# Kernel optimization log

Measured on AMD Instinct MI355X. Metric: run time of the kernel, lower is better.

## Reference

```python
import jax, jax.numpy as jnp
import numpy as np

B, S, K, D = 512, 64, 8, 16
NE, NR, NU = 2_000_000, 64, 10_000
NSTEPS, NUNITS, NITER = 100, 128, 2


def _alpha_schedule():
    # betas = sigmoid(linspace(-6,6)) * (0.005 - 1e-5) + 1e-5; alphas_prod = cumprod(1-betas)
    betas = jax.nn.sigmoid(jnp.linspace(-6.0, 6.0, NSTEPS)) * (0.005 - 1e-5) + 1e-5
    aprod = jnp.cumprod(1.0 - betas)
    return jnp.sqrt(aprod), jnp.sqrt(1.0 - aprod)


def _forward(usr_emb, ent_emb, rel_emb, agg_W, agg_b, fc1_W, fc1_b, fc2_W, fc2_b,
             mlp_W1, mlp_b1, mlp_W2, mlp_b2, mlp_W3, mlp_b3, mlp_W4, mlp_b4,
             step_emb1, step_emb2, step_emb3, noise_e, u, v, click_seq, adj_ent, adj_rel, t):
    user = usr_emb[u]                                   # [B,D]
    # --- diffusion branch: x = x0*sqrt(abar_t) + e*sqrt(1-abar_t), then MLP with step-emb adds
    abar_sqrt, ombar_sqrt = _alpha_schedule()
    x = user * abar_sqrt[t][:, None] + noise_e * ombar_sqrt[t][:, None]
    for Wl, bl, se in ((mlp_W1, mlp_b1, step_emb1), (mlp_W2, mlp_b2, step_emb2), (mlp_W3, mlp_b3, step_emb3)):
        x = jax.nn.relu(x @ Wl + bl + se[t])            # [B,128]
    diff_out = x @ mlp_W4 + mlp_b4                      # [B,D]
    # --- multi-hop neighbor gather (entities/relations per hop)
    e0 = click_seq                                      # [B,S]
    e1 = adj_ent[e0]                                    # [B,S,K]
    e2 = adj_ent[e1].reshape(B, S, K * K)               # [B,S,K*K]
    r0 = adj_rel[e0]                                    # [B,S,K]
    r1 = adj_rel[e1].reshape(B, S, K * K)               # [B,S,K*K]
    ev = [ent_emb[e0][:, :, None, :], ent_emb[e1], ent_emb[e2]]  # [B,S,1,D],[B,S,K,D],[B,S,K*K,D]
    rv = [rel_emb[r0], rel_emb[r1]]

    def aggregate(self_v, neigh_v, rel_v, act):
        # KGCN sum-aggregator: user-relation score softmax over neighbors, weighted sum, linear, act
        scores = jnp.mean(user[:, None, None, None, :] * rel_v, axis=-1)   # [B,S,n,K]
        p = jax.nn.softmax(scores, axis=-1)
        neigh_agg = jnp.einsum('bsnk,bsnkd->bsnd', p, neigh_v)             # [B,S,n,D]
        return act((self_v + neigh_agg) @ agg_W + agg_b)

    for i in range(NITER):
        act = jnp.tanh if i == NITER - 1 else jax.nn.sigmoid
        nxt = []
        for hop in range(NITER - i):
            n_self = ev[hop].shape[2]
            nv = ev[hop + 1].reshape(B, S, n_self, K, D)
            relv = rv[hop].reshape(B, S, n_self, K, D)
            nxt.append(aggregate(ev[hop], nv, relv, act))
        ev = nxt
    item_emb = jax.nn.relu(ev[0].reshape(B, S, D))      # relu applied twice in source == once
    trans = item_emb                                    # Transform treated as identity (code unavailable)
    s_sum = jax.nn.relu(jnp.sum(trans, axis=1))         # [B,D]
    s_max = jax.nn.relu(jnp.max(trans, axis=1))         # [B,D]
    fusion = jnp.concatenate([s_sum, s_max], axis=1)    # [B,2D]
    feat = jax.nn.relu(jax.nn.relu(fusion @ fc1_W + fc1_b) @ fc2_W + fc2_b)  # [B,D]
    outs = jax.nn.sigmoid(jnp.sum(feat * ent_emb[v], axis=1))               # [B]
    return jnp.concatenate([outs[:, None], diff_out], axis=1)               # [B,1+D]


def setup_inputs() -> dict:
    key = jax.random.key(0)
    ks = iter(jax.random.split(key, 32))
    nrm = lambda shape, s: jax.random.normal(next(ks), shape, dtype=jnp.float32) * s
    zf = lambda shape: jnp.zeros(shape, dtype=jnp.float32)
    ri = lambda shape, hi: jax.random.randint(next(ks), shape, 0, hi, dtype=jnp.int32)
    return {
        'usr_emb': nrm((NU, D), 0.1), 'ent_emb': nrm((NE, D), 0.1), 'rel_emb': nrm((NR, D), 0.1),
        'agg_W': nrm((D, D), 0.25), 'agg_b': zf((D,)),
        'fc1_W': nrm((2 * D, 64), 0.18), 'fc1_b': zf((64,)),
        'fc2_W': nrm((64, D), 0.125), 'fc2_b': zf((D,)),
        'mlp_W1': nrm((D, NUNITS), 0.25), 'mlp_b1': zf((NUNITS,)),
        'mlp_W2': nrm((NUNITS, NUNITS), 0.09), 'mlp_b2': zf((NUNITS,)),
        'mlp_W3': nrm((NUNITS, NUNITS), 0.09), 'mlp_b3': zf((NUNITS,)),
        'mlp_W4': nrm((NUNITS, D), 0.09), 'mlp_b4': zf((D,)),
        'step_emb1': nrm((NSTEPS, NUNITS), 0.1), 'step_emb2': nrm((NSTEPS, NUNITS), 0.1),
        'step_emb3': nrm((NSTEPS, NUNITS), 0.1),
        'noise_e': jax.random.normal(next(ks), (B, D), dtype=jnp.float32),
        'u': ri((B,), NU), 'v': ri((B,), NE), 'click_seq': ri((B, S), NE),
        'adj_ent': ri((NE, K), NE), 'adj_rel': ri((NE, K), NR), 't': ri((B,), NSTEPS),
    }


def reference(usr_emb, ent_emb, rel_emb, agg_W, agg_b, fc1_W, fc1_b, fc2_W, fc2_b,
              mlp_W1, mlp_b1, mlp_W2, mlp_b2, mlp_W3, mlp_b3, mlp_W4, mlp_b4,
              step_emb1, step_emb2, step_emb3, noise_e, u, v, click_seq, adj_ent, adj_rel, t):
    return _forward(usr_emb, ent_emb, rel_emb, agg_W, agg_b, fc1_W, fc1_b, fc2_W, fc2_b,
                    mlp_W1, mlp_b1, mlp_W2, mlp_b2, mlp_W3, mlp_b3, mlp_W4, mlp_b4,
                    step_emb1, step_emb2, step_emb3, noise_e, u, v, click_seq, adj_ent, adj_rel, t)
```

## Files before the change

kernel.cpp:

```cpp
#include <hip/hip_runtime.h>
#include <math.h>

namespace {
constexpr int B = 512, S = 64, K = 8, D = 16, NR = 64, NSTEPS = 100, NUNITS = 128;
}

__global__ void k_sched(float* __restrict__ sa, float* __restrict__ so) {
    int i = threadIdx.x;
    if (i < NSTEPS) {
        float prod = 1.0f;
        for (int jj = 0; jj <= i; ++jj) {
            float x = -6.0f + (float)jj * (12.0f / 99.0f);
            float sig = 1.0f / (1.0f + expf(-x));
            float beta = sig * (0.005f - 1e-5f) + 1e-5f;
            prod *= (1.0f - beta);
        }
        sa[i] = sqrtf(prod);
        so[i] = sqrtf(1.0f - prod);
    }
}

__global__ void k_userrel(const float* __restrict__ usr_emb,
                          const float* __restrict__ rel_emb,
                          const int* __restrict__ u,
                          float* __restrict__ w) {
    int b = blockIdx.x, r = threadIdx.x;
    const float* ur = usr_emb + (long)u[b] * D;
    const float* rr = rel_emb + r * D;
    float s = 0.f;
#pragma unroll
    for (int d = 0; d < D; ++d) s += ur[d] * rr[d];
    w[b * NR + r] = s * (1.0f / (float)D);
}

__global__ __launch_bounds__(256) void k_prep(
    const int* __restrict__ click_seq,
    const int* __restrict__ adj_ent,
    const int* __restrict__ adj_rel,
    int* __restrict__ e1s,
    int* __restrict__ r0s)
{
    int p = blockIdx.x * blockDim.x + threadIdx.x;
    int e0 = click_seq[p];
    const int4* ae = (const int4*)(adj_ent + (long)e0 * K);
    const int4* ar = (const int4*)(adj_rel + (long)e0 * K);
    int4 a0 = ae[0], a1 = ae[1];
    int4 b0 = ar[0], b1 = ar[1];
    int4* oe = (int4*)(e1s + (long)p * K);
    int4* orr = (int4*)(r0s + (long)p * K);
    oe[0] = a0; oe[1] = a1;
    orr[0] = b0; orr[1] = b1;
}

__global__ __launch_bounds__(256) void k_kgcn(
    const float* __restrict__ ent_emb,
    const float* __restrict__ w_tab,
    const int* __restrict__ click_seq,
    const int* __restrict__ adj_ent,
    const int* __restrict__ adj_rel,
    const int* __restrict__ e1s,
    const int* __restrict__ r0s,
    const float* __restrict__ agg_W,
    const float* __restrict__ agg_b,
    float* __restrict__ item)
{
    __shared__ float wb[NR];
    __shared__ float Ws[D][D + 1];
    __shared__ float bs[D];
    __shared__ float Ms[4][K][D + 1];
    __shared__ float h1s[4][K][D + 1];
    __shared__ float h0s[4][D];

    const int tid = threadIdx.x;
    const int pg = tid >> 6;
    const int lane = tid & 63;
    const int p = blockIdx.x * 4 + pg;
    const int b = blockIdx.x >> 4;

    const int k = lane >> 3, j = lane & 7;

    const int e0 = click_seq[p];
    const int e1k = e1s[(long)p * K + k];
    const int r0k = r0s[(long)p * K + k];
    const int e2kj = adj_ent[(long)e1k * K + j];
    const int r1kj = adj_rel[(long)e1k * K + j];

    Ws[tid >> 4][tid & 15] = agg_W[tid];
    if (tid < NR) wb[tid] = w_tab[b * NR + tid];
    if (tid < D) bs[tid] = agg_b[tid];
    __syncthreads();

    float s1 = wb[r1kj];
    float m1 = s1;
    m1 = fmaxf(m1, __shfl_xor(m1, 1));
    m1 = fmaxf(m1, __shfl_xor(m1, 2));
    m1 = fmaxf(m1, __shfl_xor(m1, 4));
    float ex = expf(s1 - m1);
    float den = ex;
    den += __shfl_xor(den, 1);
    den += __shfl_xor(den, 2);
    den += __shfl_xor(den, 4);
    float p1 = ex / den;

    float agg[D];
    {
        const float4* q2p = (const float4*)(ent_emb + (long)e2kj * D);
        float4 a0 = q2p[0], a1 = q2p[1], a2 = q2p[2], a3 = q2p[3];
        agg[0] = p1 * a0.x;  agg[1] = p1 * a0.y;  agg[2] = p1 * a0.z;  agg[3] = p1 * a0.w;
        agg[4] = p1 * a1.x;  agg[5] = p1 * a1.y;  agg[6] = p1 * a1.z;  agg[7] = p1 * a1.w;
        agg[8] = p1 * a2.x;  agg[9] = p1 * a2.y;  agg[10] = p1 * a2.z; agg[11] = p1 * a2.w;
        agg[12] = p1 * a3.x; agg[13] = p1 * a3.y; agg[14] = p1 * a3.z; agg[15] = p1 * a3.w;
    }
#pragma unroll
    for (int m = 1; m <= 4; m <<= 1)
#pragma unroll
        for (int d = 0; d < D; ++d) agg[d] += __shfl_xor(agg[d], m);

    float q1[D];
    {
        const float4* q1p = (const float4*)(ent_emb + (long)e1k * D);
        float4 a0 = q1p[0], a1 = q1p[1], a2 = q1p[2], a3 = q1p[3];
        q1[0] = a0.x;  q1[1] = a0.y;  q1[2] = a0.z;  q1[3] = a0.w;
        q1[4] = a1.x;  q1[5] = a1.y;  q1[6] = a1.z;  q1[7] = a1.w;
        q1[8] = a2.x;  q1[9] = a2.y;  q1[10] = a2.z; q1[11] = a2.w;
        q1[12] = a3.x; q1[13] = a3.y; q1[14] = a3.z; q1[15] = a3.w;
    }
    Ms[pg][k][2 * j]     = q1[2 * j]     + agg[2 * j];
    Ms[pg][k][2 * j + 1] = q1[2 * j + 1] + agg[2 * j + 1];
    __syncthreads();

#pragma unroll
    for (int o = lane; o < 128; o += 64) {
        int ko = o >> 4, dd = o & 15;
        float acc = bs[dd];
#pragma unroll
        for (int din = 0; din < D; ++din) acc += Ms[pg][ko][din] * Ws[din][dd];
        h1s[pg][ko][dd] = 1.0f / (1.0f + expf(-acc));
    }

    float s0 = wb[r0k];
    float m0 = s0;
    m0 = fmaxf(m0, __shfl_xor(m0, 8));
    m0 = fmaxf(m0, __shfl_xor(m0, 16));
    m0 = fmaxf(m0, __shfl_xor(m0, 32));
    float e0x = expf(s0 - m0);
    float d0 = e0x;
    d0 += __shfl_xor(d0, 8);
    d0 += __shfl_xor(d0, 16);
    d0 += __shfl_xor(d0, 32);
    float p0 = e0x / d0;

    float ag0[D];
#pragma unroll
    for (int d = 0; d < D; ++d) ag0[d] = p0 * q1[d];
#pragma unroll
    for (int m = 8; m <= 32; m <<= 1)
#pragma unroll
        for (int d = 0; d < D; ++d) ag0[d] += __shfl_xor(ag0[d], m);

    float q0v[D];
    {
        const float4* q0p = (const float4*)(ent_emb + (long)e0 * D);
        float4 a0 = q0p[0], a1 = q0p[1], a2 = q0p[2], a3 = q0p[3];
        q0v[0] = a0.x;  q0v[1] = a0.y;  q0v[2] = a0.z;  q0v[3] = a0.w;
        q0v[4] = a1.x;  q0v[5] = a1.y;  q0v[6] = a1.z;  q0v[7] = a1.w;
        q0v[8] = a2.x;  q0v[9] = a2.y;  q0v[10] = a2.z; q0v[11] = a2.w;
        q0v[12] = a3.x; q0v[13] = a3.y; q0v[14] = a3.z; q0v[15] = a3.w;
    }
    const int ddl = lane & 15;
    float acc0 = bs[ddl];
#pragma unroll
    for (int din = 0; din < D; ++din) acc0 += (q0v[din] + ag0[din]) * Ws[din][ddl];
    float h0v = 1.0f / (1.0f + expf(-acc0));
    if (lane < 16) h0s[pg][lane] = h0v;
    __syncthreads();

    float ag1[D];
#pragma unroll
    for (int d = 0; d < D; ++d) ag1[d] = p0 * h1s[pg][k][d];
#pragma unroll
    for (int m = 8; m <= 32; m <<= 1)
#pragma unroll
        for (int d = 0; d < D; ++d) ag1[d] += __shfl_xor(ag1[d], m);

    float acc1 = bs[ddl];
#pragma unroll
    for (int din = 0; din < D; ++din) acc1 += (h0s[pg][din] + ag1[din]) * Ws[din][ddl];
    float fin = tanhf(acc1);
    if (lane < 16) item[(long)p * D + lane] = fmaxf(fin, 0.0f);
}

__global__ __launch_bounds__(64) void k_fuse(
    const float* __restrict__ item,
    const float* __restrict__ fc1_W,
    const float* __restrict__ fc1_b,
    const float* __restrict__ fc2_W,
    const float* __restrict__ fc2_b,
    const float* __restrict__ ent_emb,
    const int* __restrict__ v,
    float* __restrict__ out)
{
    __shared__ float sm[S][D + 1];
    __shared__ float fus[2 * D];
    __shared__ float hid[64];
    __shared__ float feat_s[D];

    int b = blockIdx.x, t = threadIdx.x;
    const float4* ip = (const float4*)(item + ((long)b * S + t) * D);
    float4 r0 = ip[0], r1 = ip[1], r2 = ip[2], r3 = ip[3];
    sm[t][0] = r0.x;  sm[t][1] = r0.y;  sm[t][2] = r0.z;  sm[t][3] = r0.w;
    sm[t][4] = r1.x;  sm[t][5] = r1.y;  sm[t][6] = r1.z;  sm[t][7] = r1.w;
    sm[t][8] = r2.x;  sm[t][9] = r2.y;  sm[t][10] = r2.z; sm[t][11] = r2.w;
    sm[t][12] = r3.x; sm[t][13] = r3.y; sm[t][14] = r3.z; sm[t][15] = r3.w;
    __syncthreads();

    if (t < D) {
        float sv = 0.0f, mv = -1e30f;
        for (int ss = 0; ss < S; ++ss) {
            float x = sm[ss][t];
            sv += x;
            mv = fmaxf(mv, x);
        }
        fus[t] = fmaxf(sv, 0.0f);
        fus[D + t] = fmaxf(mv, 0.0f);
    }
    __syncthreads();

    float a = fc1_b[t];
#pragma unroll
    for (int i = 0; i < 2 * D; ++i) a += fus[i] * fc1_W[i * 64 + t];
    hid[t] = fmaxf(a, 0.0f);
    __syncthreads();

    if (t < D) {
        float f = fc2_b[t];
#pragma unroll
        for (int i = 0; i < 64; ++i) f += hid[i] * fc2_W[i * D + t];
        feat_s[t] = fmaxf(f, 0.0f);
    }
    __syncthreads();

    if (t < D) {
        float g = feat_s[t] * ent_emb[(long)v[b] * D + t];
        g += __shfl_xor(g, 1);
        g += __shfl_xor(g, 2);
        g += __shfl_xor(g, 4);
        g += __shfl_xor(g, 8);
        if (t == 0) out[(long)b * 17] = 1.0f / (1.0f + expf(-g));
    }
}

__global__ __launch_bounds__(128) void k_diff(
    const float* __restrict__ usr_emb, const float* __restrict__ noise_e,
    const int* __restrict__ u, const int* __restrict__ t_arr,
    const float* __restrict__ W1, const float* __restrict__ b1,
    const float* __restrict__ W2, const float* __restrict__ b2,
    const float* __restrict__ W3, const float* __restrict__ b3,
    const float* __restrict__ W4, const float* __restrict__ b4,
    const float* __restrict__ se1, const float* __restrict__ se2,
    const float* __restrict__ se3,
    const float* __restrict__ sa, const float* __restrict__ so,
    float* __restrict__ out)
{
    __shared__ float x0[D];
    __shared__ float ha[NUNITS];
    __shared__ float hb[NUNITS];

    int b = blockIdx.x, t = threadIdx.x;
    int ts = t_arr[b];
    if (t < D) {
        x0[t] = usr_emb[(long)u[b] * D + t] * sa[ts] + noise_e[(long)b * D + t] * so[ts];
    }
    __syncthreads();

    float a = b1[t] + se1[(long)ts * NUNITS + t];
#pragma unroll
    for (int i = 0; i < D; ++i) a += x0[i] * W1[i * NUNITS + t];
    ha[t] = fmaxf(a, 0.0f);
    __syncthreads();

    a = b2[t] + se2[(long)ts * NUNITS + t];
    for (int i = 0; i < NUNITS; ++i) a += ha[i] * W2[i * NUNITS + t];
    hb[t] = fmaxf(a, 0.0f);
    __syncthreads();

    a = b3[t] + se3[(long)ts * NUNITS + t];
    for (int i = 0; i < NUNITS; ++i) a += hb[i] * W3[i * NUNITS + t];
    __syncthreads();
    ha[t] = fmaxf(a, 0.0f);
    __syncthreads();

    if (t < D) {
        float acc = b4[t];
        for (int i = 0; i < NUNITS; ++i) acc += ha[i] * W4[i * D + t];
        out[(long)b * 17 + 1 + t] = acc;
    }
}

extern "C" void kernel_launch(void* const* d_in, const int* in_sizes, int n_in,
                              void* d_out, int out_size, void* d_ws, size_t ws_size,
                              hipStream_t stream) {
    const float* usr_emb = (const float*)d_in[0];
    const float* ent_emb = (const float*)d_in[1];
    const float* rel_emb = (const float*)d_in[2];
    const float* agg_W   = (const float*)d_in[3];
    const float* agg_b   = (const float*)d_in[4];
    const float* fc1_W   = (const float*)d_in[5];
    const float* fc1_b   = (const float*)d_in[6];
    const float* fc2_W   = (const float*)d_in[7];
    const float* fc2_b   = (const float*)d_in[8];
    const float* mlp_W1  = (const float*)d_in[9];
    const float* mlp_b1  = (const float*)d_in[10];
    const float* mlp_W2  = (const float*)d_in[11];
    const float* mlp_b2  = (const float*)d_in[12];
    const float* mlp_W3  = (const float*)d_in[13];
    const float* mlp_b3  = (const float*)d_in[14];
    const float* mlp_W4  = (const float*)d_in[15];
    const float* mlp_b4  = (const float*)d_in[16];
    const float* se1     = (const float*)d_in[17];
    const float* se2     = (const float*)d_in[18];
    const float* se3     = (const float*)d_in[19];
    const float* noise_e = (const float*)d_in[20];
    const int* u         = (const int*)d_in[21];
    const int* v         = (const int*)d_in[22];
    const int* click_seq = (const int*)d_in[23];
    const int* adj_ent   = (const int*)d_in[24];
    const int* adj_rel   = (const int*)d_in[25];
    const int* t         = (const int*)d_in[26];
    float* out = (float*)d_out;

    float* ws = (float*)d_ws;
    float* w_tab = ws;
    float* sa    = w_tab + B * NR;
    float* so    = sa + 128;
    float* item  = so + 128;
    int*   e1s   = (int*)(item + B * S * D);
    int*   r0s   = e1s + B * S * K;

    k_sched<<<1, 128, 0, stream>>>(sa, so);
    k_userrel<<<B, NR, 0, stream>>>(usr_emb, rel_emb, u, w_tab);
    k_prep<<<(B * S) / 256, 256, 0, stream>>>(click_seq, adj_ent, adj_rel, e1s, r0s);
    k_kgcn<<<(B * S) / 4, 256, 0, stream>>>(ent_emb, w_tab, click_seq, adj_ent, adj_rel,
                                            e1s, r0s, agg_W, agg_b, item);
    k_fuse<<<B, 64, 0, stream>>>(item, fc1_W, fc1_b, fc2_W, fc2_b, ent_emb, v, out);
    k_diff<<<B, NUNITS, 0, stream>>>(usr_emb, noise_e, u, t, mlp_W1, mlp_b1, mlp_W2, mlp_b2,
                                     mlp_W3, mlp_b3, mlp_W4, mlp_b4, se1, se2, se3, sa, so, out);
}
```

Baseline: 368.8 us.

## Fuse prep kernels and tail kernels, restructure KGCN reductions with transpose-style shuffles

Merges the schedule, user-relation and neighbor-prep kernels into one launch, and merges the fusion head with the diffusion MLP into a single tail kernel. This cuts the launch count from six to three. The KGCN kernel now uses one 64-thread block per position. Its butterfly reductions use a reduce-scatter pattern that halves the vector each step, cutting the number of shuffles. Hop-1 aggregation is now linear, computing sum p0*h1 once via shared memory instead of a 16-wide shuffle reduction. In exchange, blocks are smaller and each block reloads the weights, and there are more sync points per position.

```diff
diff --git a/kernel.cpp b/kernel.cpp
--- a/kernel.cpp
+++ b/kernel.cpp
@@ -5,54 +5,45 @@
 constexpr int B = 512, S = 64, K = 8, D = 16, NR = 64, NSTEPS = 100, NUNITS = 128;
 }
 
-__global__ void k_sched(float* __restrict__ sa, float* __restrict__ so) {
-    int i = threadIdx.x;
-    if (i < NSTEPS) {
+__global__ __launch_bounds__(256) void k_prep_all(
+    const float* __restrict__ usr_emb, const float* __restrict__ rel_emb,
+    const int* __restrict__ u, const int* __restrict__ click_seq,
+    const int* __restrict__ adj_ent, const int* __restrict__ adj_rel,
+    float* __restrict__ w_tab, int* __restrict__ e1s, int* __restrict__ r0s,
+    float* __restrict__ sa, float* __restrict__ so)
+{
+    int b = blockIdx.x, t = threadIdx.x;
+    if (t < 64) {
+        const float* ur = usr_emb + (long)u[b] * D;
+        const float* rr = rel_emb + t * D;
+        float s = 0.f;
+#pragma unroll
+        for (int d = 0; d < D; ++d) s += ur[d] * rr[d];
+        w_tab[b * NR + t] = s * (1.0f / 16.0f);
+    } else if (t < 128) {
+        int p = b * S + (t - 64);
+        int e0 = click_seq[p];
+        const int4* ae = (const int4*)(adj_ent + (long)e0 * K);
+        const int4* ar = (const int4*)(adj_rel + (long)e0 * K);
+        int4 a0 = ae[0], a1 = ae[1], b0 = ar[0], b1 = ar[1];
+        int4* oe = (int4*)(e1s + (long)p * K);
+        int4* orr = (int4*)(r0s + (long)p * K);
+        oe[0] = a0; oe[1] = a1;
+        orr[0] = b0; orr[1] = b1;
+    } else if (b == 0 && (t - 128) < NSTEPS) {
+        int i = t - 128;
         float prod = 1.0f;
         for (int jj = 0; jj <= i; ++jj) {
             float x = -6.0f + (float)jj * (12.0f / 99.0f);
             float sig = 1.0f / (1.0f + expf(-x));
-            float beta = sig * (0.005f - 1e-5f) + 1e-5f;
-            prod *= (1.0f - beta);
+            prod *= (1.0f - (sig * (0.005f - 1e-5f) + 1e-5f));
         }
         sa[i] = sqrtf(prod);
         so[i] = sqrtf(1.0f - prod);
     }
 }
 
-__global__ void k_userrel(const float* __restrict__ usr_emb,
-                          const float* __restrict__ rel_emb,
-                          const int* __restrict__ u,
-                          float* __restrict__ w) {
-    int b = blockIdx.x, r = threadIdx.x;
-    const float* ur = usr_emb + (long)u[b] * D;
-    const float* rr = rel_emb + r * D;
-    float s = 0.f;
-#pragma unroll
-    for (int d = 0; d < D; ++d) s += ur[d] * rr[d];
-    w[b * NR + r] = s * (1.0f / (float)D);
-}
-
-__global__ __launch_bounds__(256) void k_prep(
-    const int* __restrict__ click_seq,
-    const int* __restrict__ adj_ent,
-    const int* __restrict__ adj_rel,
-    int* __restrict__ e1s,
-    int* __restrict__ r0s)
-{
-    int p = blockIdx.x * blockDim.x + threadIdx.x;
-    int e0 = click_seq[p];
-    const int4* ae = (const int4*)(adj_ent + (long)e0 * K);
-    const int4* ar = (const int4*)(adj_rel + (long)e0 * K);
-    int4 a0 = ae[0], a1 = ae[1];
-    int4 b0 = ar[0], b1 = ar[1];
-    int4* oe = (int4*)(e1s + (long)p * K);
-    int4* orr = (int4*)(r0s + (long)p * K);
-    oe[0] = a0; oe[1] = a1;
-    orr[0] = b0; orr[1] = b1;
-}
-
-__global__ __launch_bounds__(256) void k_kgcn(
+__global__ __launch_bounds__(64) void k_kgcn(
     const float* __restrict__ ent_emb,
     const float* __restrict__ w_tab,
     const int* __restrict__ click_seq,
@@ -67,16 +58,16 @@
     __shared__ float wb[NR];
     __shared__ float Ws[D][D + 1];
     __shared__ float bs[D];
-    __shared__ float Ms[4][K][D + 1];
-    __shared__ float h1s[4][K][D + 1];
-    __shared__ float h0s[4][D];
-
-    const int tid = threadIdx.x;
-    const int pg = tid >> 6;
-    const int lane = tid & 63;
-    const int p = blockIdx.x * 4 + pg;
-    const int b = blockIdx.x >> 4;
-
+    __shared__ float Ms[K][D + 1];
+    __shared__ float h1s[K][D + 1];
+    __shared__ float h0s[D];
+    __shared__ float A0s[D];
+    __shared__ float M1s[D];
+    __shared__ float p0s[K];
+
+    const int lane = threadIdx.x;
+    const int p = blockIdx.x;
+    const int b = p >> 6;
     const int k = lane >> 3, j = lane & 7;
 
     const int e0 = click_seq[p];
@@ -85,9 +76,14 @@
     const int e2kj = adj_ent[(long)e1k * K + j];
     const int r1kj = adj_rel[(long)e1k * K + j];
 
-    Ws[tid >> 4][tid & 15] = agg_W[tid];
-    if (tid < NR) wb[tid] = w_tab[b * NR + tid];
-    if (tid < D) bs[tid] = agg_b[tid];
+    {
+        const float4 wv = ((const float4*)agg_W)[lane];
+        int row = lane >> 2, col = (lane & 3) * 4;
+        Ws[row][col] = wv.x; Ws[row][col + 1] = wv.y;
+        Ws[row][col + 2] = wv.z; Ws[row][col + 3] = wv.w;
+        wb[lane] = w_tab[b * NR + lane];
+        if (lane < D) bs[lane] = agg_b[lane];
+    }
     __syncthreads();
 
     float s1 = wb[r1kj];
@@ -102,40 +98,56 @@
     den += __shfl_xor(den, 4);
     float p1 = ex / den;
 
-    float agg[D];
+    float q2r[D], q1r[D], q0r[D];
     {
         const float4* q2p = (const float4*)(ent_emb + (long)e2kj * D);
         float4 a0 = q2p[0], a1 = q2p[1], a2 = q2p[2], a3 = q2p[3];
-        agg[0] = p1 * a0.x;  agg[1] = p1 * a0.y;  agg[2] = p1 * a0.z;  agg[3] = p1 * a0.w;
-        agg[4] = p1 * a1.x;  agg[5] = p1 * a1.y;  agg[6] = p1 * a1.z;  agg[7] = p1 * a1.w;
-        agg[8] = p1 * a2.x;  agg[9] = p1 * a2.y;  agg[10] = p1 * a2.z; agg[11] = p1 * a2.w;
-        agg[12] = p1 * a3.x; agg[13] = p1 * a3.y; agg[14] = p1 * a3.z; agg[15] = p1 * a3.w;
-    }
-#pragma unroll
-    for (int m = 1; m <= 4; m <<= 1)
-#pragma unroll
-        for (int d = 0; d < D; ++d) agg[d] += __shfl_xor(agg[d], m);
-
-    float q1[D];
+        q2r[0]=a0.x; q2r[1]=a0.y; q2r[2]=a0.z; q2r[3]=a0.w;
+        q2r[4]=a1.x; q2r[5]=a1.y; q2r[6]=a1.z; q2r[7]=a1.w;
+        q2r[8]=a2.x; q2r[9]=a2.y; q2r[10]=a2.z; q2r[11]=a2.w;
+        q2r[12]=a3.x; q2r[13]=a3.y; q2r[14]=a3.z; q2r[15]=a3.w;
+    }
     {
         const float4* q1p = (const float4*)(ent_emb + (long)e1k * D);
         float4 a0 = q1p[0], a1 = q1p[1], a2 = q1p[2], a3 = q1p[3];
-        q1[0] = a0.x;  q1[1] = a0.y;  q1[2] = a0.z;  q1[3] = a0.w;
-        q1[4] = a1.x;  q1[5] = a1.y;  q1[6] = a1.z;  q1[7] = a1.w;
-        q1[8] = a2.x;  q1[9] = a2.y;  q1[10] = a2.z; q1[11] = a2.w;
-        q1[12] = a3.x; q1[13] = a3.y; q1[14] = a3.z; q1[15] = a3.w;
-    }
-    Ms[pg][k][2 * j]     = q1[2 * j]     + agg[2 * j];
-    Ms[pg][k][2 * j + 1] = q1[2 * j + 1] + agg[2 * j + 1];
-    __syncthreads();
-
-#pragma unroll
-    for (int o = lane; o < 128; o += 64) {
-        int ko = o >> 4, dd = o & 15;
-        float acc = bs[dd];
-#pragma unroll
-        for (int din = 0; din < D; ++din) acc += Ms[pg][ko][din] * Ws[din][dd];
-        h1s[pg][ko][dd] = 1.0f / (1.0f + expf(-acc));
+        q1r[0]=a0.x; q1r[1]=a0.y; q1r[2]=a0.z; q1r[3]=a0.w;
+        q1r[4]=a1.x; q1r[5]=a1.y; q1r[6]=a1.z; q1r[7]=a1.w;
+        q1r[8]=a2.x; q1r[9]=a2.y; q1r[10]=a2.z; q1r[11]=a2.w;
+        q1r[12]=a3.x; q1r[13]=a3.y; q1r[14]=a3.z; q1r[15]=a3.w;
+    }
+    {
+        const float4* q0p = (const float4*)(ent_emb + (long)e0 * D);
+        float4 a0 = q0p[0], a1 = q0p[1], a2 = q0p[2], a3 = q0p[3];
+        q0r[0]=a0.x; q0r[1]=a0.y; q0r[2]=a0.z; q0r[3]=a0.w;
+        q0r[4]=a1.x; q0r[5]=a1.y; q0r[6]=a1.z; q0r[7]=a1.w;
+        q0r[8]=a2.x; q0r[9]=a2.y; q0r[10]=a2.z; q0r[11]=a2.w;
+        q0r[12]=a3.x; q0r[13]=a3.y; q0r[14]=a3.z; q0r[15]=a3.w;
+    }
+
+    {
+        float cur[16];
+#pragma unroll
+        for (int d = 0; d < 16; ++d) cur[d] = p1 * q2r[d];
+        const bool b0 = (lane & 1), b1 = (lane & 2), b2 = (lane & 4);
+        float n8[8];
+#pragma unroll
+        for (int d = 0; d < 8; ++d) {
+            float snd = b0 ? cur[d] : cur[d + 8];
+            float kp  = b0 ? cur[d + 8] : cur[d];
+            n8[d] = kp + __shfl_xor(snd, 1);
+        }
+        float n4[4];
+#pragma unroll
+        for (int d = 0; d < 4; ++d) {
+            float snd = b1 ? n8[d] : n8[d + 4];
+            float kp  = b1 ? n8[d + 4] : n8[d];
+            n4[d] = kp + __shfl_xor(snd, 2);
+        }
+        float a0 = (b2 ? n4[2] : n4[0]) + __shfl_xor(b2 ? n4[0] : n4[2], 4);
+        float a1 = (b2 ? n4[3] : n4[1]) + __shfl_xor(b2 ? n4[1] : n4[3], 4);
+        const int dbase = (b0 ? 8 : 0) + (b1 ? 4 : 0) + (b2 ? 2 : 0);
+        Ms[k][dbase]     = q1r[dbase]     + a0;
+        Ms[k][dbase + 1] = q1r[dbase + 1] + a1;
     }
 
     float s0 = wb[r0k];
@@ -149,108 +161,74 @@
     d0 += __shfl_xor(d0, 16);
     d0 += __shfl_xor(d0, 32);
     float p0 = e0x / d0;
-
-    float ag0[D];
-#pragma unroll
-    for (int d = 0; d < D; ++d) ag0[d] = p0 * q1[d];
-#pragma unroll
-    for (int m = 8; m <= 32; m <<= 1)
-#pragma unroll
-        for (int d = 0; d < D; ++d) ag0[d] += __shfl_xor(ag0[d], m);
-
-    float q0v[D];
-    {
-        const float4* q0p = (const float4*)(ent_emb + (long)e0 * D);
-        float4 a0 = q0p[0], a1 = q0p[1], a2 = q0p[2], a3 = q0p[3];
-        q0v[0] = a0.x;  q0v[1] = a0.y;  q0v[2] = a0.z;  q0v[3] = a0.w;
-        q0v[4] = a1.x;  q0v[5] = a1.y;  q0v[6] = a1.z;  q0v[7] = a1.w;
-        q0v[8] = a2.x;  q0v[9] = a2.y;  q0v[10] = a2.z; q0v[11] = a2.w;
-        q0v[12] = a3.x; q0v[13] = a3.y; q0v[14] = a3.z; q0v[15] = a3.w;
-    }
+    if (j == 0) p0s[k] = p0;
+
+    {
+        float cur[16];
+#pragma unroll
+        for (int d = 0; d < 16; ++d) cur[d] = p0 * q1r[d];
+        const bool c0 = (lane & 8), c1 = (lane & 16), c2 = (lane & 32);
+        float n8[8];
+#pragma unroll
+        for (int d = 0; d < 8; ++d) {
+            float snd = c0 ? cur[d] : cur[d + 8];
+            float kp  = c0 ? cur[d + 8] : cur[d];
+            n8[d] = kp + __shfl_xor(snd, 8);
+        }
+        float n4[4];
+#pragma unroll
+        for (int d = 0; d < 4; ++d) {
+            float snd = c1 ? n8[d] : n8[d + 4];
+            float kp  = c1 ? n8[d + 4] : n8[d];
+            n4[d] = kp + __shfl_xor(snd, 16);
+        }
+        float a0 = (c2 ? n4[2] : n4[0]) + __shfl_xor(c2 ? n4[0] : n4[2], 32);
+        float a1 = (c2 ? n4[3] : n4[1]) + __shfl_xor(c2 ? n4[1] : n4[3], 32);
+        const int dbase = (c0 ? 8 : 0) + (c1 ? 4 : 0) + (c2 ? 2 : 0);
+        if (j == 0) { A0s[dbase] = a0; A0s[dbase + 1] = a1; }
+    }
+    __syncthreads();
+
+#pragma unroll
+    for (int o = lane; o < 128; o += 64) {
+        int ko = o >> 4, dd = o & 15;
+        float acc = bs[dd];
+#pragma unroll
+        for (int din = 0; din < D; ++din) acc += Ms[ko][din] * Ws[din][dd];
+        h1s[ko][dd] = 1.0f / (1.0f + expf(-acc));
+    }
+
     const int ddl = lane & 15;
-    float acc0 = bs[ddl];
-#pragma unroll
-    for (int din = 0; din < D; ++din) acc0 += (q0v[din] + ag0[din]) * Ws[din][ddl];
-    float h0v = 1.0f / (1.0f + expf(-acc0));
-    if (lane < 16) h0s[pg][lane] = h0v;
-    __syncthreads();
-
-    float ag1[D];
-#pragma unroll
-    for (int d = 0; d < D; ++d) ag1[d] = p0 * h1s[pg][k][d];
-#pragma unroll
-    for (int m = 8; m <= 32; m <<= 1)
-#pragma unroll
-        for (int d = 0; d < D; ++d) ag1[d] += __shfl_xor(ag1[d], m);
-
-    float acc1 = bs[ddl];
-#pragma unroll
-    for (int din = 0; din < D; ++din) acc1 += (h0s[pg][din] + ag1[din]) * Ws[din][ddl];
-    float fin = tanhf(acc1);
-    if (lane < 16) item[(long)p * D + lane] = fmaxf(fin, 0.0f);
-}
-
-__global__ __launch_bounds__(64) void k_fuse(
+    {
+        float acc = bs[ddl];
+#pragma unroll
+        for (int din = 0; din < D; ++din)
+            acc += (q0r[din] + A0s[din]) * Ws[din][ddl];
+        if (lane < D) h0s[lane] = 1.0f / (1.0f + expf(-acc));
+    }
+    __syncthreads();
+
+    if (lane < D) {
+        float m = h0s[lane];
+#pragma unroll
+        for (int kk = 0; kk < K; ++kk) m += p0s[kk] * h1s[kk][lane];
+        M1s[lane] = m;
+    }
+    __syncthreads();
+
+    {
+        float acc = bs[ddl];
+#pragma unroll
+        for (int din = 0; din < D; ++din) acc += M1s[din] * Ws[din][ddl];
+        if (lane < D) item[(long)p * D + lane] = fmaxf(tanhf(acc), 0.0f);
+    }
+}
+
+__global__ __launch_bounds__(128) void k_tail(
     const float* __restrict__ item,
-    const float* __restrict__ fc1_W,
-    const float* __restrict__ fc1_b,
-    const float* __restrict__ fc2_W,
-    const float* __restrict__ fc2_b,
-    const float* __restrict__ ent_emb,
-    const int* __restrict__ v,
-    float* __restrict__ out)
-{
-    __shared__ float sm[S][D + 1];
-    __shared__ float fus[2 * D];
-    __shared__ float hid[64];
-    __shared__ float feat_s[D];
-
-    int b = blockIdx.x, t = threadIdx.x;
-    const float4* ip = (const float4*)(item + ((long)b * S + t) * D);
-    float4 r0 = ip[0], r1 = ip[1], r2 = ip[2], r3 = ip[3];
-    sm[t][0] = r0.x;  sm[t][1] = r0.y;  sm[t][2] = r0.z;  sm[t][3] = r0.w;
-    sm[t][4] = r1.x;  sm[t][5] = r1.y;  sm[t][6] = r1.z;  sm[t][7] = r1.w;
-    sm[t][8] = r2.x;  sm[t][9] = r2.y;  sm[t][10] = r2.z; sm[t][11] = r2.w;
-    sm[t][12] = r3.x; sm[t][13] = r3.y; sm[t][14] = r3.z; sm[t][15] = r3.w;
-    __syncthreads();
-
-    if (t < D) {
-        float sv = 0.0f, mv = -1e30f;
-        for (int ss = 0; ss < S; ++ss) {
-            float x = sm[ss][t];
-            sv += x;
-            mv = fmaxf(mv, x);
-        }
-        fus[t] = fmaxf(sv, 0.0f);
-        fus[D + t] = fmaxf(mv, 0.0f);
-    }
-    __syncthreads();
-
-    float a = fc1_b[t];
-#pragma unroll
-    for (int i = 0; i < 2 * D; ++i) a += fus[i] * fc1_W[i * 64 + t];
-    hid[t] = fmaxf(a, 0.0f);
-    __syncthreads();
-
-    if (t < D) {
-        float f = fc2_b[t];
-#pragma unroll
-        for (int i = 0; i < 64; ++i) f += hid[i] * fc2_W[i * D + t];
-        feat_s[t] = fmaxf(f, 0.0f);
-    }
-    __syncthreads();
-
-    if (t < D) {
-        float g = feat_s[t] * ent_emb[(long)v[b] * D + t];
-        g += __shfl_xor(g, 1);
-        g += __shfl_xor(g, 2);
-        g += __shfl_xor(g, 4);
-        g += __shfl_xor(g, 8);
-        if (t == 0) out[(long)b * 17] = 1.0f / (1.0f + expf(-g));
-    }
-}
-
-__global__ __launch_bounds__(128) void k_diff(
+    const float* __restrict__ fc1_W, const float* __restrict__ fc1_b,
+    const float* __restrict__ fc2_W, const float* __restrict__ fc2_b,
+    const float* __restrict__ ent_emb, const int* __restrict__ v,
     const float* __restrict__ usr_emb, const float* __restrict__ noise_e,
     const int* __restrict__ u, const int* __restrict__ t_arr,
     const float* __restrict__ W1, const float* __restrict__ b1,
@@ -265,12 +243,16 @@
     __shared__ float x0[D];
     __shared__ float ha[NUNITS];
     __shared__ float hb[NUNITS];
+    __shared__ float sm[S][D + 1];
+    __shared__ float fus[2 * D];
+    __shared__ float hid[64];
+    __shared__ float feat_s[D];
 
     int b = blockIdx.x, t = threadIdx.x;
     int ts = t_arr[b];
-    if (t < D) {
+
+    if (t < D)
         x0[t] = usr_emb[(long)u[b] * D + t] * sa[ts] + noise_e[(long)b * D + t] * so[ts];
-    }
     __syncthreads();
 
     float a = b1[t] + se1[(long)ts * NUNITS + t];
@@ -294,6 +276,53 @@
         float acc = b4[t];
         for (int i = 0; i < NUNITS; ++i) acc += ha[i] * W4[i * D + t];
         out[(long)b * 17 + 1 + t] = acc;
+    }
+
+    if (t < 64) {
+        const float4* ip = (const float4*)(item + ((long)b * S + t) * D);
+        float4 r0 = ip[0], r1 = ip[1], r2 = ip[2], r3 = ip[3];
+        sm[t][0]=r0.x;  sm[t][1]=r0.y;  sm[t][2]=r0.z;  sm[t][3]=r0.w;
+        sm[t][4]=r1.x;  sm[t][5]=r1.y;  sm[t][6]=r1.z;  sm[t][7]=r1.w;
+        sm[t][8]=r2.x;  sm[t][9]=r2.y;  sm[t][10]=r2.z; sm[t][11]=r2.w;
+        sm[t][12]=r3.x; sm[t][13]=r3.y; sm[t][14]=r3.z; sm[t][15]=r3.w;
+    }
+    __syncthreads();
+
+    if (t < D) {
+        float sv = 0.0f, mv = -1e30f;
+        for (int ss = 0; ss < S; ++ss) {
+            float x = sm[ss][t];
+            sv += x;
+            mv = fmaxf(mv, x);
+        }
+        fus[t] = fmaxf(sv, 0.0f);
+        fus[D + t] = fmaxf(mv, 0.0f);
+    }
+    __syncthreads();
+
+    if (t < 64) {
+        float acc = fc1_b[t];
+#pragma unroll
+        for (int i = 0; i < 2 * D; ++i) acc += fus[i] * fc1_W[i * 64 + t];
+        hid[t] = fmaxf(acc, 0.0f);
+    }
+    __syncthreads();
+
+    if (t < D) {
+        float f = fc2_b[t];
+#pragma unroll
+        for (int i = 0; i < 64; ++i) f += hid[i] * fc2_W[i * D + t];
+        feat_s[t] = fmaxf(f, 0.0f);
+    }
+    __syncthreads();
+
+    if (t < D) {
+        float g = feat_s[t] * ent_emb[(long)v[b] * D + t];
+        g += __shfl_xor(g, 1);
+        g += __shfl_xor(g, 2);
+        g += __shfl_xor(g, 4);
+        g += __shfl_xor(g, 8);
+        if (t == 0) out[(long)b * 17] = 1.0f / (1.0f + expf(-g));
     }
 }
 
@@ -337,12 +366,11 @@
     int*   e1s   = (int*)(item + B * S * D);
     int*   r0s   = e1s + B * S * K;
 
-    k_sched<<<1, 128, 0, stream>>>(sa, so);
-    k_userrel<<<B, NR, 0, stream>>>(usr_emb, rel_emb, u, w_tab);
-    k_prep<<<(B * S) / 256, 256, 0, stream>>>(click_seq, adj_ent, adj_rel, e1s, r0s);
-    k_kgcn<<<(B * S) / 4, 256, 0, stream>>>(ent_emb, w_tab, click_seq, adj_ent, adj_rel,
-                                            e1s, r0s, agg_W, agg_b, item);
-    k_fuse<<<B, 64, 0, stream>>>(item, fc1_W, fc1_b, fc2_W, fc2_b, ent_emb, v, out);
-    k_diff<<<B, NUNITS, 0, stream>>>(usr_emb, noise_e, u, t, mlp_W1, mlp_b1, mlp_W2, mlp_b2,
-                                     mlp_W3, mlp_b3, mlp_W4, mlp_b4, se1, se2, se3, sa, so, out);
-}
+    k_prep_all<<<B, 256, 0, stream>>>(usr_emb, rel_emb, u, click_seq, adj_ent, adj_rel,
+                                      w_tab, e1s, r0s, sa, so);
+    k_kgcn<<<B * S, 64, 0, stream>>>(ent_emb, w_tab, click_seq, adj_ent, adj_rel,
+                                     e1s, r0s, agg_W, agg_b, item);
+    k_tail<<<B, 128, 0, stream>>>(item, fc1_W, fc1_b, fc2_W, fc2_b, ent_emb, v,
+                                  usr_emb, noise_e, u, t, mlp_W1, mlp_b1, mlp_W2, mlp_b2,
+                                  mlp_W3, mlp_b3, mlp_W4, mlp_b4, se1, se2, se3, sa, so, out);
+}
```

Measured after the change: 339.7 us. 1.09x faster.
